# Optimization experiments

Measured on AMD Instinct MI355X. Metric: run time of the kernel, lower is better.

Reference implementation:

```python
import jax, jax.numpy as jnp
import numpy as np

EPS = 1e-5
HEADS = 8
KSIZE = (3, 3, 3)
DIL = (1, 1, 1)


def _nbr_idx(L, k, d):
    # NATTEN-style border-clamped neighborhood start indices. [L, k]
    i = jnp.arange(L)
    start = jnp.clip(i - (k // 2) * d, 0, L - (k - 1) * d - 1)
    return start[:, None] + d * jnp.arange(k)[None, :]


def _inorm(x):
    # InstanceNorm3d (affine=False): normalize over D,H,W per (B,C). x: [B,C,D,H,W]
    m = x.mean(axis=(2, 3, 4), keepdims=True)
    v = x.var(axis=(2, 3, 4), keepdims=True)
    return (x - m) * jax.lax.rsqrt(v + EPS)


def _gather_nbrs(x, idD, idH, idW):
    # x: [B,D,H,W,C] -> [B,D,H,W,kd,kh,kw,C]
    B, D, H, W, C = x.shape
    kd, kh, kw = idD.shape[1], idH.shape[1], idW.shape[1]
    g = jnp.take(x, idD.reshape(-1), axis=1).reshape(B, D, kd, H, W, C)
    g = jnp.take(g, idH.reshape(-1), axis=3).reshape(B, D, kd, H, kh, W, C)
    g = jnp.take(g, idW.reshape(-1), axis=5).reshape(B, D, kd, H, kh, W, kw, C)
    return g.transpose(0, 1, 3, 5, 2, 4, 6, 7)


def setup_inputs() -> dict:
    key = jax.random.key(0)
    ks = jax.random.split(key, 8)
    B, C, D, H, W = 1, 64, 64, 64, 8
    kd, kh, kw = KSIZE
    n = lambda k, s: jax.random.normal(k, s, dtype=jnp.float32)
    return {
        "skip": n(ks[0], (B, C, D, H, W)),
        "up": n(ks[1], (B, C, D, H, W)),
        "w_qk": n(ks[2], (C, 2 * C)) * 0.05,
        "b_qk": jnp.zeros((2 * C,), jnp.float32),
        "w_v": n(ks[3], (C, C)) * 0.05,
        "b_v": jnp.zeros((C,), jnp.float32),
        "w_proj": n(ks[4], (C, C)) * 0.05,
        "b_proj": jnp.zeros((C,), jnp.float32),
        "rpb": n(ks[5], (HEADS, 2 * kd - 1, 2 * kh - 1, 2 * kw - 1)) * 0.02,
    }


def reference(skip, up, w_qk, b_qk, w_v, b_v, w_proj, b_proj, rpb):
    B, C, D, H, W = skip.shape
    kd, kh, kw = KSIZE
    dd, dh, dw = DIL
    hd = C // HEADS
    scale = hd ** -0.5

    up_n = _inorm(up)
    skip_n = _inorm(skip)

    x_qk = skip_n.transpose(0, 2, 3, 4, 1)  # [B,D,H,W,C]
    x_v = up_n.transpose(0, 2, 3, 4, 1)

    qk = x_qk @ w_qk + b_qk              # [B,D,H,W,2C]
    q, k = jnp.split(qk, 2, axis=-1)
    v = x_v @ w_v + b_v                  # [B,D,H,W,C]

    idD = _nbr_idx(D, kd, dd)
    idH = _nbr_idx(H, kh, dh)
    idW = _nbr_idx(W, kw, dw)

    K3 = kd * kh * kw
    kn = _gather_nbrs(k, idD, idH, idW).reshape(B, D, H, W, K3, HEADS, hd)
    vn = _gather_nbrs(v, idD, idH, idW).reshape(B, D, H, W, K3, HEADS, hd)
    qh = q.reshape(B, D, H, W, HEADS, hd)

    # relative position bias lookup: [HEADS, D, H, W, kd, kh, kw]
    relD = (idD - jnp.arange(D)[:, None]) // dd + (kd - 1)
    relH = (idH - jnp.arange(H)[:, None]) // dh + (kh - 1)
    relW = (idW - jnp.arange(W)[:, None]) // dw + (kw - 1)
    bias = rpb[:,
               relD[:, None, None, :, None, None],
               relH[None, :, None, None, :, None],
               relW[None, None, :, None, None, :]]
    bias = bias.reshape(HEADS, D, H, W, K3).transpose(1, 2, 3, 0, 4)  # [D,H,W,h,K3]

    logits = jnp.einsum('bxyzhd,bxyzkhd->bxyzhk', qh, kn) * scale + bias[None]
    attn = jax.nn.softmax(logits, axis=-1)
    out = jnp.einsum('bxyzhk,bxyzkhd->bxyzhd', attn, vn).reshape(B, D, H, W, C)
    out = out @ w_proj + b_proj
    return out.transpose(0, 4, 1, 2, 3)  # [B,C,D,H,W]
```

## Files before the change

kernel.cpp:

```cpp
#include <hip/hip_runtime.h>
#include <hip/hip_bf16.h>
#include <math.h>


#define PD 64
#define PH 64
#define PW 8
#define PTOT (PD*PH*PW)
#define NC 64
#define NHEADS 8
#define HD 8
#define ATT_SCALE 0.35355339059327373f

#define WS_MR   0
#define WS_Q16  1024
#define WS_K16  (WS_Q16 + PTOT*32)
#define WS_V16  (WS_K16 + PTOT*32)

__device__ __forceinline__ void unpack8(uint4 u, float f[8]) {
  union { unsigned int i; float x; } a;
  a.i = u.x << 16;          f[0] = a.x;
  a.i = u.x & 0xffff0000u;  f[1] = a.x;
  a.i = u.y << 16;          f[2] = a.x;
  a.i = u.y & 0xffff0000u;  f[3] = a.x;
  a.i = u.z << 16;          f[4] = a.x;
  a.i = u.z & 0xffff0000u;  f[5] = a.x;
  a.i = u.w << 16;          f[6] = a.x;
  a.i = u.w & 0xffff0000u;  f[7] = a.x;
}

__device__ __forceinline__ uint4 shfl4(uint4 v, int src) {
  uint4 r;
  r.x = (unsigned)__shfl((int)v.x, src, 64);
  r.y = (unsigned)__shfl((int)v.y, src, 64);
  r.z = (unsigned)__shfl((int)v.z, src, 64);
  r.w = (unsigned)__shfl((int)v.w, src, 64);
  return r;
}

__global__ __launch_bounds__(1024) void k_stats(const float* __restrict__ skip,
                                                const float* __restrict__ up,
                                                float* __restrict__ ws) {
  int tc = blockIdx.x;
  const float* src = (tc < 64) ? (skip + (size_t)tc * PTOT)
                               : (up + (size_t)(tc - 64) * PTOT);
  const float4* b4 = (const float4*)src;
  float s1 = 0.f, s2 = 0.f;
  #pragma unroll
  for (int it = 0; it < 8; it++) {
    float4 v = b4[it * 1024 + threadIdx.x];
    s1 += v.x + v.y + v.z + v.w;
    s2 += v.x*v.x + v.y*v.y + v.z*v.z + v.w*v.w;
  }
  #pragma unroll
  for (int off = 32; off; off >>= 1) {
    s1 += __shfl_down(s1, off);
    s2 += __shfl_down(s2, off);
  }
  __shared__ float red[32];
  int wid = threadIdx.x >> 6;
  if ((threadIdx.x & 63) == 0) { red[wid*2] = s1; red[wid*2+1] = s2; }
  __syncthreads();
  if (threadIdx.x == 0) {
    float a = 0.f, b = 0.f;
    #pragma unroll
    for (int w2 = 0; w2 < 16; w2++) { a += red[w2*2]; b += red[w2*2+1]; }
    float mean = a / (float)PTOT;
    float var  = b / (float)PTOT - mean*mean;
    ws[WS_MR + tc*2]     = mean;
    ws[WS_MR + tc*2 + 1] = rsqrtf(var + 1e-5f);
  }
}

__global__ __launch_bounds__(256) void k_qkv(const float* __restrict__ skip,
                                             const float* __restrict__ up,
                                             const float* __restrict__ w_qk,
                                             const float* __restrict__ b_qk,
                                             const float* __restrict__ w_v,
                                             const float* __restrict__ b_v,
                                             float* __restrict__ ws) {
  int lane = threadIdx.x & 63;
  int wid  = threadIdx.x >> 6;
  int cs = __builtin_amdgcn_readfirstlane(blockIdx.y * 4 + wid);
  int bidx = ((blockIdx.x & 7) << 6) + (blockIdx.x >> 3);
  int p  = bidx * 64 + lane;
  const float* mr = ws + WS_MR;
  unsigned short* q16 = (unsigned short*)(ws + WS_Q16);
  unsigned short* k16 = (unsigned short*)(ws + WS_K16);
  unsigned short* v16 = (unsigned short*)(ws + WS_V16);
  float acc[16];
  unsigned short* base;
  int jbl;
  if (cs < 8) {
    int jb = cs * 16;
    #pragma unroll
    for (int j = 0; j < 16; j++) acc[j] = b_qk[jb + j];
    const float* w = w_qk + jb;
    #pragma unroll 8
    for (int c = 0; c < NC; c++) {
      float a = (skip[(size_t)c * PTOT + p] - mr[c*2]) * mr[c*2+1];
      #pragma unroll
      for (int j = 0; j < 16; j++)
        acc[j] = fmaf(a, w[c*128 + j], acc[j]);
    }
    base = (jb < 64) ? q16 : k16;
    jbl = jb & 63;
  } else {
    int jb = (cs - 8) * 16;
    #pragma unroll
    for (int j = 0; j < 16; j++) acc[j] = b_v[jb + j];
    const float* w = w_v + jb;
    #pragma unroll 8
    for (int c = 0; c < NC; c++) {
      float a = (up[(size_t)c * PTOT + p] - mr[128 + c*2]) * mr[128 + c*2+1];
      #pragma unroll
      for (int j = 0; j < 16; j++)
        acc[j] = fmaf(a, w[c*64 + j], acc[j]);
    }
    base = v16;
    jbl = jb;
  }
  unsigned short t[16];
  #pragma unroll
  for (int j = 0; j < 16; j++) {
    __hip_bfloat16 b = __float2bfloat16(acc[j]);
    t[j] = *reinterpret_cast<unsigned short*>(&b);
  }
  unsigned short* dst = base + (size_t)(p >> 3) * 512 + (jbl >> 3) * 64 + (p & 7) * 8;
  *(uint4*)(dst)      = *(const uint4*)(t);
  *(uint4*)(dst + 64) = *(const uint4*)(t + 8);
}

__global__ __launch_bounds__(512) void k_attn_proj(const float* __restrict__ rpb,
                                                   const float* __restrict__ w_proj,
                                                   const float* __restrict__ b_proj,
                                                   float* __restrict__ ws,
                                                   float* __restrict__ out) {
  __shared__ float A[64][65];
  __shared__ float rpb_s[NHEADS * 125];
  for (int i = threadIdx.x; i < NHEADS*125; i += 512) rpb_s[i] = rpb[i];
  __syncthreads();

  int bid = ((blockIdx.x & 7) << 6) + (blockIdx.x >> 3);

  int wid  = threadIdx.x >> 6;
  int lane = threadIdx.x & 63;
  int job = bid * 8 + wid;
  int d = job >> 6;
  int h = job & 63;
  int w    = lane >> 3;
  int head = lane & 7;

  int sd = min(max(d - 1, 0), PD - 3);
  int sh = min(max(h - 1, 0), PH - 3);
  int sw = min(max(w - 1, 0), PW - 3);

  const unsigned short* q16 = (const unsigned short*)(ws + WS_Q16);
  const unsigned short* k16 = (const unsigned short*)(ws + WS_K16);
  const unsigned short* v16 = (const unsigned short*)(ws + WS_V16);

  int dh = (d << 6) + h;
  uint4 qw = *(const uint4*)(q16 + (size_t)dh * 512 + head * 64 + w * 8);
  float qv[8];
  unpack8(qw, qv);
  int hb = head * 125;
  int bb0 = hb + (sd - d + 2) * 25 + (sh - h + 2) * 5 + (sw - w + 2);
  int src0 = (head << 3) + sw;

  float den = 0.f;
  float av[8] = {0,0,0,0,0,0,0,0};

  uint4 kC, vC, kA, vA, kB, vB;
  {
    size_t o0 = (size_t)((sd << 6) + sh) * 512;
    size_t o1 = (size_t)((sd << 6) + sh + 1) * 512;
    kC = ((const uint4*)(k16 + o0))[lane];
    vC = ((const uint4*)(v16 + o0))[lane];
    kA = ((const uint4*)(k16 + o1))[lane];
    vA = ((const uint4*)(v16 + o1))[lane];
  }

  int jdc = 0, jhc = 0;
  int jd2 = 0, jh2 = 2;
  #pragma unroll 1
  for (int g = 0; g < 9; g++) {
    if (g < 7) {
      size_t o = (size_t)(((sd + jd2) << 6) + (sh + jh2)) * 512;
      kB = ((const uint4*)(k16 + o))[lane];
      vB = ((const uint4*)(v16 + o))[lane];
      jh2++; if (jh2 == 3) { jh2 = 0; jd2++; }
    }
    int bb = bb0 + jdc * 25 + jhc * 5;
    jhc++; if (jhc == 3) { jhc = 0; jdc++; }

    #pragma unroll
    for (int t = 0; t < 3; t++) {
      uint4 kw = shfl4(kC, src0 + t);
      uint4 vw = shfl4(vC, src0 + t);
      float kv[8];
      unpack8(kw, kv);
      float dot = qv[0]*kv[0] + qv[1]*kv[1] + qv[2]*kv[2] + qv[3]*kv[3]
                + qv[4]*kv[4] + qv[5]*kv[5] + qv[6]*kv[6] + qv[7]*kv[7];
      float l = dot * ATT_SCALE + rpb_s[bb + t];
      float pp = __expf(l);
      den += pp;
      float vv[8];
      unpack8(vw, vv);
      #pragma unroll
      for (int i = 0; i < 8; i++) av[i] = fmaf(pp, vv[i], av[i]);
    }
    kC = kA; vC = vA;
    kA = kB; vA = vB;
  }
  float inv = 1.f / den;

  int pl = wid * 8 + w;
  int cb = head * 8;
  #pragma unroll
  for (int i = 0; i < 8; i++)
    A[pl][cb + i] = av[i] * inv;
  __syncthreads();

  int jb = __builtin_amdgcn_readfirstlane(wid * 8);
  int p0 = bid * 64;
  float acc[8];
  #pragma unroll
  for (int j = 0; j < 8; j++) acc[j] = b_proj[jb + j];
  #pragma unroll 8
  for (int c = 0; c < NC; c++) {
    float a = A[lane][c];
    #pragma unroll
    for (int j = 0; j < 8; j++)
      acc[j] = fmaf(a, w_proj[c*64 + jb + j], acc[j]);
  }
  #pragma unroll
  for (int j = 0; j < 8; j++)
    out[(size_t)(jb + j) * PTOT + p0 + lane] = acc[j];
}

extern "C" void kernel_launch(void* const* d_in, const int* in_sizes, int n_in,
                              void* d_out, int out_size, void* d_ws, size_t ws_size,
                              hipStream_t stream) {
  const float* skip = (const float*)d_in[0];
  const float* up   = (const float*)d_in[1];
  const float* w_qk = (const float*)d_in[2];
  const float* b_qk = (const float*)d_in[3];
  const float* w_v  = (const float*)d_in[4];
  const float* b_v  = (const float*)d_in[5];
  const float* w_pr = (const float*)d_in[6];
  const float* b_pr = (const float*)d_in[7];
  const float* rpb  = (const float*)d_in[8];
  float* ws  = (float*)d_ws;
  float* out = (float*)d_out;

  k_stats<<<128, 1024, 0, stream>>>(skip, up, ws);
  k_qkv<<<dim3(512, 3), 256, 0, stream>>>(skip, up, w_qk, b_qk, w_v, b_v, ws);
  k_attn_proj<<<(PD*PH)/8, 512, 0, stream>>>(rpb, w_pr, b_pr, ws, out);
}
```

Baseline: 43.65 us.

## Compute QKV projection with bf16 MFMA and shared-memory staging in one block per tile

The QKV projection kernel now stages the normalized skip and up activations plus all weights as bf16 in shared memory, then computes the 64x192 output tile with 16x16x32 bf16 MFMA instructions. The result goes through LDS and is written out in the packed q/k/v layout. This removes the 3x re-reading of activations across the y-grid and the scalar FMA loop. In exchange each block converts the full weight matrix every launch, and the inputs are rounded to bf16 before the matmul, which lowers precision.

```diff
diff --git a/kernel.cpp b/kernel.cpp
--- a/kernel.cpp
+++ b/kernel.cpp
@@ -16,6 +16,14 @@
 #define WS_Q16  1024
 #define WS_K16  (WS_Q16 + PTOT*32)
 #define WS_V16  (WS_K16 + PTOT*32)
+
+typedef short short8 __attribute__((ext_vector_type(8)));
+typedef float f32x4 __attribute__((ext_vector_type(4)));
+
+__device__ __forceinline__ unsigned short bf16bits(float x) {
+  __hip_bfloat16 b = __float2bfloat16(x);
+  return *reinterpret_cast<unsigned short*>(&b);
+}
 
 __device__ __forceinline__ void unpack8(uint4 u, float f[8]) {
   union { unsigned int i; float x; } a;
@@ -79,56 +87,77 @@
                                              const float* __restrict__ w_v,
                                              const float* __restrict__ b_v,
                                              float* __restrict__ ws) {
-  int lane = threadIdx.x & 63;
-  int wid  = threadIdx.x >> 6;
-  int cs = __builtin_amdgcn_readfirstlane(blockIdx.y * 4 + wid);
+  __shared__ __align__(16) short Wf[12*2*64*8];
+  __shared__ __align__(16) short As[64*72];
+  __shared__ __align__(16) short Au[64*72];
+  __shared__ __align__(16) short Cl[64*200];
+
+  int tid = threadIdx.x;
   int bidx = ((blockIdx.x & 7) << 6) + (blockIdx.x >> 3);
-  int p  = bidx * 64 + lane;
+  int p0 = bidx * 64;
   const float* mr = ws + WS_MR;
+
+  #pragma unroll
+  for (int it = 0; it < 16; it++) {
+    int idx = tid + it * 256;
+    int c = idx >> 6, pl = idx & 63;
+    float xs = skip[(size_t)c * PTOT + p0 + pl];
+    float xu = up  [(size_t)c * PTOT + p0 + pl];
+    As[pl*72 + c] = (short)bf16bits((xs - mr[c*2])       * mr[c*2+1]);
+    Au[pl*72 + c] = (short)bf16bits((xu - mr[128 + c*2]) * mr[128 + c*2+1]);
+  }
+  #pragma unroll
+  for (int it = 0; it < 48; it++) {
+    int e = tid + it * 256;
+    int i = e & 7, l = (e >> 3) & 63, kh = (e >> 9) & 1, jt = e >> 10;
+    int k = kh*32 + ((l >> 4) << 3) + i;
+    int j = jt*16 + (l & 15);
+    float wv_ = (j < 128) ? w_qk[k*128 + j] : w_v[k*64 + (j - 128)];
+    Wf[e] = (short)bf16bits(wv_);
+  }
+  __syncthreads();
+
+  int wid = tid >> 6, l = tid & 63;
+  int prow = wid*16 + (l & 15);
+  short8 a_s0 = *(const short8*)&As[prow*72 + 0  + ((l>>4)<<3)];
+  short8 a_s1 = *(const short8*)&As[prow*72 + 32 + ((l>>4)<<3)];
+  short8 a_u0 = *(const short8*)&Au[prow*72 + 0  + ((l>>4)<<3)];
+  short8 a_u1 = *(const short8*)&Au[prow*72 + 32 + ((l>>4)<<3)];
+  #pragma unroll
+  for (int jt = 0; jt < 12; jt++) {
+    float b = (jt < 8) ? b_qk[jt*16 + (l&15)] : b_v[(jt-8)*16 + (l&15)];
+    f32x4 acc = {b, b, b, b};
+    short8 b0 = *(const short8*)&Wf[((jt*2 + 0)*64 + l)*8];
+    short8 b1 = *(const short8*)&Wf[((jt*2 + 1)*64 + l)*8];
+    if (jt < 8) {
+      acc = __builtin_amdgcn_mfma_f32_16x16x32_bf16(a_s0, b0, acc, 0, 0, 0);
+      acc = __builtin_amdgcn_mfma_f32_16x16x32_bf16(a_s1, b1, acc, 0, 0, 0);
+    } else {
+      acc = __builtin_amdgcn_mfma_f32_16x16x32_bf16(a_u0, b0, acc, 0, 0, 0);
+      acc = __builtin_amdgcn_mfma_f32_16x16x32_bf16(a_u1, b1, acc, 0, 0, 0);
+    }
+    #pragma unroll
+    for (int i2 = 0; i2 < 4; i2++) {
+      int r = ((l >> 4) << 2) + i2;
+      Cl[(wid*16 + r)*200 + jt*16 + (l & 15)] = (short)bf16bits(acc[i2]);
+    }
+  }
+  __syncthreads();
+
   unsigned short* q16 = (unsigned short*)(ws + WS_Q16);
   unsigned short* k16 = (unsigned short*)(ws + WS_K16);
   unsigned short* v16 = (unsigned short*)(ws + WS_V16);
-  float acc[16];
-  unsigned short* base;
-  int jbl;
-  if (cs < 8) {
-    int jb = cs * 16;
-    #pragma unroll
-    for (int j = 0; j < 16; j++) acc[j] = b_qk[jb + j];
-    const float* w = w_qk + jb;
-    #pragma unroll 8
-    for (int c = 0; c < NC; c++) {
-      float a = (skip[(size_t)c * PTOT + p] - mr[c*2]) * mr[c*2+1];
-      #pragma unroll
-      for (int j = 0; j < 16; j++)
-        acc[j] = fmaf(a, w[c*128 + j], acc[j]);
-    }
-    base = (jb < 64) ? q16 : k16;
-    jbl = jb & 63;
-  } else {
-    int jb = (cs - 8) * 16;
-    #pragma unroll
-    for (int j = 0; j < 16; j++) acc[j] = b_v[jb + j];
-    const float* w = w_v + jb;
-    #pragma unroll 8
-    for (int c = 0; c < NC; c++) {
-      float a = (up[(size_t)c * PTOT + p] - mr[128 + c*2]) * mr[128 + c*2+1];
-      #pragma unroll
-      for (int j = 0; j < 16; j++)
-        acc[j] = fmaf(a, w[c*64 + j], acc[j]);
-    }
-    base = v16;
-    jbl = jb;
-  }
-  unsigned short t[16];
-  #pragma unroll
-  for (int j = 0; j < 16; j++) {
-    __hip_bfloat16 b = __float2bfloat16(acc[j]);
-    t[j] = *reinterpret_cast<unsigned short*>(&b);
-  }
-  unsigned short* dst = base + (size_t)(p >> 3) * 512 + (jbl >> 3) * 64 + (p & 7) * 8;
-  *(uint4*)(dst)      = *(const uint4*)(t);
-  *(uint4*)(dst + 64) = *(const uint4*)(t + 8);
+  #pragma unroll
+  for (int it = 0; it < 6; it++) {
+    int ch = tid + it * 256;
+    int pl = ch & 63, hj = ch >> 6;
+    short8 v8 = *(const short8*)&Cl[pl*200 + hj*8];
+    int p = p0 + pl;
+    unsigned short* baseT = (hj < 8) ? q16 : (hj < 16) ? k16 : v16;
+    int head = hj & 7;
+    unsigned short* dst = baseT + (size_t)(p >> 3)*512 + head*64 + (p & 7)*8;
+    *(uint4*)dst = *(const uint4*)&v8;
+  }
 }
 
 __global__ __launch_bounds__(512) void k_attn_proj(const float* __restrict__ rpb,
@@ -254,6 +283,6 @@
   float* out = (float*)d_out;
 
   k_stats<<<128, 1024, 0, stream>>>(skip, up, ws);
-  k_qkv<<<dim3(512, 3), 256, 0, stream>>>(skip, up, w_qk, b_qk, w_v, b_v, ws);
+  k_qkv<<<512, 256, 0, stream>>>(skip, up, w_qk, b_qk, w_v, b_v, ws);
   k_attn_proj<<<(PD*PH)/8, 512, 0, stream>>>(rpb, w_pr, b_pr, ws, out);
 }
```

New measurement: 42.68 us. -2.2%, faster.
